# Kernel tuning notes

Hardware: AMD Instinct MI355X
Metric: run time of the kernel (lower is better)

Reference implementation:

```python
import jax, jax.numpy as jnp
import numpy as np

B, T, DIM, H, KV, HD = 1, 2048, 2048, 16, 4, 128


def _rope_tables(T, hd):
    half = hd // 2
    inv_freq = 1.0 / (10000.0 ** (np.arange(0, half, dtype=np.float32) / half))
    t = np.arange(T, dtype=np.float32)
    freqs = np.outer(t, inv_freq)                # [T, hd/2]
    emb = np.concatenate([freqs, freqs], axis=-1)  # [T, hd]
    return jnp.asarray(np.cos(emb)), jnp.asarray(np.sin(emb))


def setup_inputs() -> dict:
    key = jax.random.key(0)
    kx, kq, kk, kv, ko = jax.random.split(key, 5)
    s = 0.02
    x = jax.random.normal(kx, (B, T, DIM), dtype=jnp.float32)
    wq = jax.random.normal(kq, (H * HD, DIM), dtype=jnp.float32) * s
    wk = jax.random.normal(kk, (KV * HD, DIM), dtype=jnp.float32) * s
    wv = jax.random.normal(kv, (KV * HD, DIM), dtype=jnp.float32) * s
    wo = jax.random.normal(ko, (DIM, H * HD), dtype=jnp.float32) * s
    cos, sin = _rope_tables(T, HD)
    return {"x": x, "wq": wq, "wk": wk, "wv": wv, "wo": wo, "cos": cos, "sin": sin}


def _rotate_half(u):
    u1, u2 = jnp.split(u, 2, axis=-1)
    return jnp.concatenate([-u2, u1], axis=-1)


def _apply_rope(u, cos, sin):
    # u: [B, T, h, hd]; cos/sin: [T, hd]
    c = cos[None, :, None, :]
    s = sin[None, :, None, :]
    return u * c + _rotate_half(u) * s


def reference(x, wq, wk, wv, wo, cos, sin):
    b, t, dim = x.shape
    hd = cos.shape[1]
    h = wq.shape[0] // hd
    kvh = wk.shape[0] // hd
    rep = h // kvh
    scale = hd ** -0.5

    q = (x @ wq.T).reshape(b, t, h, hd)
    k = (x @ wk.T).reshape(b, t, kvh, hd)
    v = (x @ wv.T).reshape(b, t, kvh, hd)

    q = _apply_rope(q, cos, sin)
    k = _apply_rope(k, cos, sin)

    # Group queries by shared KV head instead of materializing repeat_kv
    qg = q.reshape(b, t, kvh, rep, hd)
    scores = jnp.einsum('bqgrd,bkgd->bgrqk', qg, k) * scale  # [b,g,r,T,T]
    causal = jnp.tril(jnp.ones((t, t), dtype=bool))
    scores = jnp.where(causal[None, None, None], scores, jnp.float32(-1e30))
    attn = jax.nn.softmax(scores, axis=-1)
    out = jnp.einsum('bgrqk,bkgd->bqgrd', attn, v).reshape(b, t, h * hd)
    return out @ wo.T
```

## Files before the change

### kernel.cpp

```cpp
#include <hip/hip_runtime.h>
#include <hip/hip_bf16.h>

typedef unsigned short u16;
typedef __attribute__((ext_vector_type(8))) short bf16x8;
typedef __attribute__((ext_vector_type(4))) float f32x4;

#define T_SEQ 2048
#define DIM   2048
#define NH    16
#define NKV   4
#define HD    128
#define NQKV  3072
#define SCALE 0.08838834764831845f
#define CHUNK 512

__device__ __forceinline__ u16 f2bf(float f) {
  unsigned int u = __float_as_uint(f);
  unsigned int r = (u + 0x7fffu + ((u >> 16) & 1u)) >> 16;
  return (u16)r;
}
__device__ __forceinline__ float bf2f(u16 v) {
  return __uint_as_float(((unsigned int)v) << 16);
}

#define B1 1048576
#define B2 2097152
#define B3 2359296
#define B4 2621440
#define B5 3670016
__global__ void cast_all(const float4* __restrict__ x,  const float4* __restrict__ wq,
                         const float4* __restrict__ wk, const float4* __restrict__ wv,
                         const float4* __restrict__ wo,
                         ushort4* __restrict__ xb, ushort4* __restrict__ wqkvb,
                         ushort4* __restrict__ wob) {
  int i = blockIdx.x * 256 + threadIdx.x;
  const float4* src; ushort4* dst; int j;
  if (i < B1)      { src = x;  dst = xb;               j = i; }
  else if (i < B2) { src = wq; dst = wqkvb;            j = i - B1; }
  else if (i < B3) { src = wk; dst = wqkvb + 1048576;  j = i - B2; }
  else if (i < B4) { src = wv; dst = wqkvb + 1310720;  j = i - B3; }
  else             { src = wo; dst = wob;              j = i - B4; }
  float4 v = src[j];
  ushort4 o;
  o.x = f2bf(v.x); o.y = f2bf(v.y); o.z = f2bf(v.z); o.w = f2bf(v.w);
  dst[j] = o;
}

#define BM 128
#define BN 128
#define BK 64
#define LDP 72

__global__ __launch_bounds__(256) void gemm_bt(
    const u16* __restrict__ A, const u16* __restrict__ W,
    float* __restrict__ Cf, u16* __restrict__ Cb, int M, int N, int K)
{
  __shared__ u16 As[BM * LDP];
  __shared__ u16 Bs[BN * LDP];
  const int tid  = threadIdx.x;
  const int lane = tid & 63;
  const int wave = tid >> 6;
  const int ln   = lane & 15;
  const int quad = lane >> 4;
  const int m0 = blockIdx.y * BM;
  const int n0 = blockIdx.x * BN;
  const int wm = (wave >> 1) * 64;
  const int wn = (wave & 1) * 64;

  const int sr = tid >> 3;
  const int sc = (tid & 7) * 8;

  f32x4 acc[4][4] = {};

  for (int k0 = 0; k0 < K; k0 += BK) {
#pragma unroll
    for (int c = 0; c < 4; ++c) {
      int row = c * 32 + sr;
      *(bf16x8*)&As[row * LDP + sc] =
          *(const bf16x8*)&A[(size_t)(m0 + row) * K + k0 + sc];
      *(bf16x8*)&Bs[row * LDP + sc] =
          *(const bf16x8*)&W[(size_t)(n0 + row) * K + k0 + sc];
    }
    __syncthreads();
#pragma unroll
    for (int ks = 0; ks < 2; ++ks) {
      bf16x8 af[4], bfr[4];
#pragma unroll
      for (int mt = 0; mt < 4; ++mt)
        af[mt] = *(const bf16x8*)&As[(wm + mt * 16 + ln) * LDP + ks * 32 + quad * 8];
#pragma unroll
      for (int nt = 0; nt < 4; ++nt)
        bfr[nt] = *(const bf16x8*)&Bs[(wn + nt * 16 + ln) * LDP + ks * 32 + quad * 8];
#pragma unroll
      for (int mt = 0; mt < 4; ++mt)
#pragma unroll
        for (int nt = 0; nt < 4; ++nt)
          acc[mt][nt] = __builtin_amdgcn_mfma_f32_16x16x32_bf16(
              af[mt], bfr[nt], acc[mt][nt], 0, 0, 0);
    }
    __syncthreads();
  }

#pragma unroll
  for (int mt = 0; mt < 4; ++mt)
#pragma unroll
    for (int nt = 0; nt < 4; ++nt)
#pragma unroll
      for (int r = 0; r < 4; ++r) {
        int row = m0 + wm + mt * 16 + quad * 4 + r;
        int col = n0 + wn + nt * 16 + ln;
        if (Cb) Cb[(size_t)row * N + col] = f2bf(acc[mt][nt][r]);
        else    Cf[(size_t)row * N + col] = acc[mt][nt][r];
      }
}

__global__ void rope_fused(const u16* __restrict__ QKVb,
                           const float* __restrict__ cosT,
                           const float* __restrict__ sinT,
                           u16* __restrict__ Qs, u16* __restrict__ Kb,
                           u16* __restrict__ Vt)
{
  int b = blockIdx.x, d = threadIdx.x;
  if (b < T_SEQ * NH) {
    int t = b >> 4;
    int h = b & 15;
    const u16* row = QKVb + (size_t)t * NQKV + h * HD;
    float u = bf2f(row[d]);
    float pr = (d < 64) ? -bf2f(row[d + 64]) : bf2f(row[d - 64]);
    float c = cosT[t * HD + d], s = sinT[t * HD + d];
    Qs[(size_t)b * HD + d] = f2bf((u * c + pr * s) * SCALE);
  } else if (b < T_SEQ * (NH + NKV)) {
    int b2 = b - T_SEQ * NH;
    int t = b2 >> 2;
    int g = b2 & 3;
    const u16* row = QKVb + (size_t)t * NQKV + DIM + g * HD;
    float u = bf2f(row[d]);
    float pr = (d < 64) ? -bf2f(row[d + 64]) : bf2f(row[d - 64]);
    float c = cosT[t * HD + d], s = sinT[t * HD + d];
    Kb[(size_t)b2 * HD + d] = f2bf(u * c + pr * s);
  } else {
    int b3 = b - T_SEQ * (NH + NKV);
    int idx = b3 * 128 + d;
    int t  = idx & (T_SEQ - 1);
    int dd = (idx >> 11) & (HD - 1);
    int g  = idx >> 18;
    Vt[idx] = QKVb[(size_t)t * NQKV + DIM + NKV * HD + g * HD + dd];
  }
}

#define KSP 136
#define VSP 72
#define PSP 72
__global__ __launch_bounds__(256) void flash_partial(
    const u16* __restrict__ Qs, const u16* __restrict__ Kb,
    const u16* __restrict__ Vt, u16* __restrict__ Opart,
    float* __restrict__ lpart)
{
  const int c  = blockIdx.x;
  const int qi = blockIdx.y;
  const int h  = blockIdx.z;
  const int b  = qi >> 2;
  if (c > b) return;
  const int g  = h >> 2;
  const int q0 = qi << 7;
  const int k0 = c << 9;
  const int kend = min(k0 + CHUNK, q0 + 128);

  __shared__ u16 Ks[64 * KSP];
  __shared__ u16 Vs[HD * VSP];
  __shared__ u16 Ps[4][16 * PSP];

  const int tid  = threadIdx.x;
  const int lane = tid & 63;
  const int w    = tid >> 6;
  const int ln   = lane & 15;
  const int quad = lane >> 4;

  bf16x8 aq[2][4];
#pragma unroll
  for (int mt = 0; mt < 2; ++mt) {
    const u16* qp = Qs + ((size_t)(q0 + w * 32 + mt * 16 + ln) * NH + h) * HD + quad * 8;
#pragma unroll
    for (int ks = 0; ks < 4; ++ks) aq[mt][ks] = *(const bf16x8*)&qp[ks * 32];
  }

  f32x4 o[2][8] = {};
  float rs[2][4] = {};

  for (int jb = k0; jb < kend; jb += 64) {
    {
      int r = tid >> 4, cc = (tid & 15) * 8;
#pragma unroll
      for (int i = 0; i < 4; ++i) {
        int row = i * 16 + r;
        *(bf16x8*)&Ks[row * KSP + cc] =
            *(const bf16x8*)&Kb[((size_t)(jb + row) * NKV + g) * HD + cc];
      }
    }
    {
      int r = tid >> 3, cc = (tid & 7) * 8;
#pragma unroll
      for (int i = 0; i < 4; ++i) {
        int row = i * 32 + r;
        *(bf16x8*)&Vs[row * VSP + cc] =
            *(const bf16x8*)&Vt[(size_t)(g * HD + row) * T_SEQ + jb + cc];
      }
    }
    __syncthreads();

#pragma unroll
    for (int mt = 0; mt < 2; ++mt) {
      const int rbase = q0 + w * 32 + mt * 16 + quad * 4;
      const int rmax  = q0 + w * 32 + mt * 16 + 15;
      if (jb <= rmax) {
        f32x4 sc[4];
#pragma unroll
        for (int nb = 0; nb < 4; ++nb) {
          f32x4 s = {};
#pragma unroll
          for (int ks = 0; ks < 4; ++ks) {
            bf16x8 kf = *(const bf16x8*)&Ks[(nb * 16 + ln) * KSP + ks * 32 + quad * 8];
            s = __builtin_amdgcn_mfma_f32_16x16x32_bf16(aq[mt][ks], kf, s, 0, 0, 0);
          }
          sc[nb] = s;
        }
        const bool diag = (jb >= q0);
#pragma unroll
        for (int nb = 0; nb < 4; ++nb) {
          int j = jb + nb * 16 + ln;
#pragma unroll
          for (int r = 0; r < 4; ++r) {
            float p = (!diag || j <= rbase + r) ? __expf(sc[nb][r]) : 0.f;
            rs[mt][r] += p;
            Ps[w][(quad * 4 + r) * PSP + nb * 16 + ln] = f2bf(p);
          }
        }
#pragma unroll
        for (int kst = 0; kst < 2; ++kst) {
          bf16x8 ap = *(const bf16x8*)&Ps[w][ln * PSP + kst * 32 + quad * 8];
#pragma unroll
          for (int nb8 = 0; nb8 < 8; ++nb8) {
            bf16x8 bv = *(const bf16x8*)&Vs[(nb8 * 16 + ln) * VSP + kst * 32 + quad * 8];
            o[mt][nb8] = __builtin_amdgcn_mfma_f32_16x16x32_bf16(ap, bv, o[mt][nb8], 0, 0, 0);
          }
        }
      }
    }
    __syncthreads();
  }

  const int slot = h * 40 + 2 * b * (b + 1) + (qi & 3) * (b + 1) + c;
  u16*   op = Opart + (size_t)slot * (128 * 128);
  float* lp = lpart + (size_t)slot * 128;
#pragma unroll
  for (int mt = 0; mt < 2; ++mt) {
#pragma unroll
    for (int r = 0; r < 4; ++r)
#pragma unroll
      for (int off = 1; off < 16; off <<= 1)
        rs[mt][r] += __shfl_xor(rs[mt][r], off);
    int rowb = w * 32 + mt * 16 + quad * 4;
#pragma unroll
    for (int r = 0; r < 4; ++r) {
#pragma unroll
      for (int nb8 = 0; nb8 < 8; ++nb8)
        op[(rowb + r) * 128 + nb8 * 16 + ln] = f2bf(o[mt][nb8][r]);
      if (ln == 0) lp[rowb + r] = rs[mt][r];
    }
  }
}

__global__ void flash_reduce(const u16* __restrict__ Opart,
                             const float* __restrict__ lpart,
                             u16* __restrict__ AO)
{
  const int h = blockIdx.y;
  const int d = threadIdx.x & 127;
  const int t = blockIdx.x * 2 + (threadIdx.x >> 7);
  const int qi = t >> 7, r = t & 127;
  const int b = qi >> 2;
  const int base = h * 40 + 2 * b * (b + 1) + (qi & 3) * (b + 1);
  float so = 0.f, sl = 0.f;
  for (int cc = 0; cc <= b; ++cc) {
    so += bf2f(Opart[(size_t)(base + cc) * (128 * 128) + r * 128 + d]);
    sl += lpart[(size_t)(base + cc) * 128 + r];
  }
  AO[(size_t)t * DIM + h * HD + d] = f2bf(so / sl);
}

extern "C" void kernel_launch(void* const* d_in, const int* in_sizes, int n_in,
                              void* d_out, int out_size, void* d_ws, size_t ws_size,
                              hipStream_t stream) {
  const float* x    = (const float*)d_in[0];
  const float* wq   = (const float*)d_in[1];
  const float* wk   = (const float*)d_in[2];
  const float* wv   = (const float*)d_in[3];
  const float* wo   = (const float*)d_in[4];
  const float* cosT = (const float*)d_in[5];
  const float* sinT = (const float*)d_in[6];
  float* out = (float*)d_out;

  char* ws = (char*)d_ws;
  const size_t MB = 1024 * 1024;
  u16*   xb    = (u16*)(ws + 0 * MB);
  u16*   wqkvb = (u16*)(ws + 8 * MB);
  u16*   wob   = (u16*)(ws + 20 * MB);
  u16*   QKVb  = (u16*)(ws + 28 * MB);
  u16*   Qs    = (u16*)(ws + 8 * MB);
  u16*   Kb    = (u16*)(ws + 16 * MB);
  u16*   Vt    = (u16*)(ws + 18 * MB);
  u16*   AO    = (u16*)(ws + 0 * MB);
  u16*   Opart = (u16*)(ws + 28 * MB);
  float* lpart = (float*)(ws + 48 * MB);

  cast_all<<<B5 / 256, 256, 0, stream>>>(
      (const float4*)x, (const float4*)wq, (const float4*)wk, (const float4*)wv,
      (const float4*)wo, (ushort4*)xb, (ushort4*)wqkvb, (ushort4*)wob);

  gemm_bt<<<dim3(NQKV / BN, T_SEQ / BM), 256, 0, stream>>>(
      xb, wqkvb, nullptr, QKVb, T_SEQ, NQKV, DIM);

  rope_fused<<<T_SEQ * (NH + NKV) + (NKV * HD * T_SEQ) / 128, HD, 0, stream>>>(
      QKVb, cosT, sinT, Qs, Kb, Vt);

  flash_partial<<<dim3(4, 16, 16), 256, 0, stream>>>(Qs, Kb, Vt, Opart, lpart);
  flash_reduce<<<dim3(T_SEQ / 2, NH), 256, 0, stream>>>(Opart, lpart, AO);

  gemm_bt<<<dim3(DIM / BN, T_SEQ / BM), 256, 0, stream>>>(
      AO, wob, out, nullptr, T_SEQ, DIM, DIM);
}
```

Measured before the change: 286.5 us.

## Balance flash-attention splits, swizzle LDS layouts, use direct global-to-LDS GEMM loads

Replaces the fixed 512-key chunking of flash attention with a per-query-tile variable split (61 slots per head, heaviest tiles scheduled first) so that work items are more even and no blocks exit early. K, V and P shared-memory tiles switch from padded rows to XOR-swizzled layouts to avoid bank conflicts. The GEMM stages its tiles with global_load_lds straight into unpadded LDS. The wo cast is split into a separate kernel placed after the QKV GEMM, and workspace offsets are reshuffled, which adds a launch and risks bank conflicts in the now unpadded GEMM LDS reads.

```diff
diff --git a/kernel.cpp b/kernel.cpp
--- a/kernel.cpp
+++ b/kernel.cpp
@@ -12,7 +12,7 @@
 #define HD    128
 #define NQKV  3072
 #define SCALE 0.08838834764831845f
-#define CHUNK 512
+#define NSLOT 61
 
 __device__ __forceinline__ u16 f2bf(float f) {
   unsigned int u = __float_as_uint(f);
@@ -22,41 +22,48 @@
 __device__ __forceinline__ float bf2f(u16 v) {
   return __uint_as_float(((unsigned int)v) << 16);
 }
-
-#define B1 1048576
-#define B2 2097152
-#define B3 2359296
-#define B4 2621440
-#define B5 3670016
-__global__ void cast_all(const float4* __restrict__ x,  const float4* __restrict__ wq,
-                         const float4* __restrict__ wk, const float4* __restrict__ wv,
-                         const float4* __restrict__ wo,
-                         ushort4* __restrict__ xb, ushort4* __restrict__ wqkvb,
-                         ushort4* __restrict__ wob) {
+__device__ __forceinline__ void gload_lds16(const u16* g, u16* l) {
+  __builtin_amdgcn_global_load_lds(
+      (const __attribute__((address_space(1))) unsigned int*)g,
+      (__attribute__((address_space(3))) unsigned int*)l, 16, 0, 0);
+}
+
+#define C1 1048576
+#define C2 2097152
+#define C3 2359296
+#define C4 2621440
+__global__ void cast_main(const float4* __restrict__ x,  const float4* __restrict__ wq,
+                          const float4* __restrict__ wk, const float4* __restrict__ wv,
+                          ushort4* __restrict__ xb, ushort4* __restrict__ wqkvb) {
   int i = blockIdx.x * 256 + threadIdx.x;
   const float4* src; ushort4* dst; int j;
-  if (i < B1)      { src = x;  dst = xb;               j = i; }
-  else if (i < B2) { src = wq; dst = wqkvb;            j = i - B1; }
-  else if (i < B3) { src = wk; dst = wqkvb + 1048576;  j = i - B2; }
-  else if (i < B4) { src = wv; dst = wqkvb + 1310720;  j = i - B3; }
-  else             { src = wo; dst = wob;              j = i - B4; }
+  if (i < C1)      { src = x;  dst = xb;               j = i; }
+  else if (i < C2) { src = wq; dst = wqkvb;            j = i - C1; }
+  else if (i < C3) { src = wk; dst = wqkvb + 1048576;  j = i - C2; }
+  else             { src = wv; dst = wqkvb + 1310720;  j = i - C3; }
   float4 v = src[j];
   ushort4 o;
   o.x = f2bf(v.x); o.y = f2bf(v.y); o.z = f2bf(v.z); o.w = f2bf(v.w);
   dst[j] = o;
 }
+__global__ void cast_wo(const float4* __restrict__ wo, ushort4* __restrict__ wob) {
+  int i = blockIdx.x * 256 + threadIdx.x;
+  float4 v = wo[i];
+  ushort4 o;
+  o.x = f2bf(v.x); o.y = f2bf(v.y); o.z = f2bf(v.z); o.w = f2bf(v.w);
+  wob[i] = o;
+}
 
 #define BM 128
 #define BN 128
 #define BK 64
-#define LDP 72
 
 __global__ __launch_bounds__(256) void gemm_bt(
     const u16* __restrict__ A, const u16* __restrict__ W,
     float* __restrict__ Cf, u16* __restrict__ Cb, int M, int N, int K)
 {
-  __shared__ u16 As[BM * LDP];
-  __shared__ u16 Bs[BN * LDP];
+  __shared__ u16 As[BM * BK];
+  __shared__ u16 Bs[BN * BK];
   const int tid  = threadIdx.x;
   const int lane = tid & 63;
   const int wave = tid >> 6;
@@ -67,19 +74,20 @@
   const int wm = (wave >> 1) * 64;
   const int wn = (wave & 1) * 64;
 
-  const int sr = tid >> 3;
-  const int sc = (tid & 7) * 8;
+  const int srow = wave * 32 + (lane >> 3);
+  const int scol = (lane & 7) * 8;
+  const u16* ga = A + (size_t)(m0 + srow) * K + scol;
+  const u16* gw = W + (size_t)(n0 + srow) * K + scol;
+  u16* la = &As[wave * 32 * BK];
+  u16* lb = &Bs[wave * 32 * BK];
 
   f32x4 acc[4][4] = {};
 
   for (int k0 = 0; k0 < K; k0 += BK) {
 #pragma unroll
-    for (int c = 0; c < 4; ++c) {
-      int row = c * 32 + sr;
-      *(bf16x8*)&As[row * LDP + sc] =
-          *(const bf16x8*)&A[(size_t)(m0 + row) * K + k0 + sc];
-      *(bf16x8*)&Bs[row * LDP + sc] =
-          *(const bf16x8*)&W[(size_t)(n0 + row) * K + k0 + sc];
+    for (int i = 0; i < 4; ++i) {
+      gload_lds16(ga + k0 + (size_t)(i * 8) * K, la + i * 8 * BK);
+      gload_lds16(gw + k0 + (size_t)(i * 8) * K, lb + i * 8 * BK);
     }
     __syncthreads();
 #pragma unroll
@@ -87,10 +95,10 @@
       bf16x8 af[4], bfr[4];
 #pragma unroll
       for (int mt = 0; mt < 4; ++mt)
-        af[mt] = *(const bf16x8*)&As[(wm + mt * 16 + ln) * LDP + ks * 32 + quad * 8];
+        af[mt] = *(const bf16x8*)&As[(wm + mt * 16 + ln) * BK + ks * 32 + quad * 8];
 #pragma unroll
       for (int nt = 0; nt < 4; ++nt)
-        bfr[nt] = *(const bf16x8*)&Bs[(wn + nt * 16 + ln) * LDP + ks * 32 + quad * 8];
+        bfr[nt] = *(const bf16x8*)&Bs[(wn + nt * 16 + ln) * BK + ks * 32 + quad * 8];
 #pragma unroll
       for (int mt = 0; mt < 4; ++mt)
 #pragma unroll
@@ -148,33 +156,48 @@
   }
 }
 
-#define KSP 136
-#define VSP 72
-#define PSP 72
 __global__ __launch_bounds__(256) void flash_partial(
     const u16* __restrict__ Qs, const u16* __restrict__ Kb,
     const u16* __restrict__ Vt, u16* __restrict__ Opart,
     float* __restrict__ lpart)
 {
-  const int c  = blockIdx.x;
-  const int qi = blockIdx.y;
-  const int h  = blockIdx.z;
-  const int b  = qi >> 2;
-  if (c > b) return;
+  __shared__ u16 Ks[64 * 128];
+  __shared__ u16 Vs[128 * 64];
+  __shared__ u16 Ps[4][16 * 64];
+
+  const int srev = 60 - (int)blockIdx.x;
+  const int h = blockIdx.y;
+  int qi, c;
+  if      (srev >= 54) { qi = 15; c = srev - 54; }
+  else if (srev >= 48) { qi = 14; c = srev - 48; }
+  else if (srev >= 42) { qi = 13; c = srev - 42; }
+  else if (srev >= 36) { qi = 12; c = srev - 36; }
+  else if (srev >= 31) { qi = 11; c = srev - 31; }
+  else if (srev >= 26) { qi = 10; c = srev - 26; }
+  else if (srev >= 22) { qi = 9;  c = srev - 22; }
+  else if (srev >= 18) { qi = 8;  c = srev - 18; }
+  else if (srev >= 14) { qi = 7;  c = srev - 14; }
+  else if (srev >= 11) { qi = 6;  c = srev - 11; }
+  else if (srev >= 8)  { qi = 5;  c = srev - 8; }
+  else if (srev >= 6)  { qi = 4;  c = srev - 6; }
+  else if (srev >= 4)  { qi = 3;  c = srev - 4; }
+  else if (srev >= 2)  { qi = 2;  c = srev - 2; }
+  else                 { qi = srev; c = 0; }
+
+  const int nt   = 2 * (qi + 1);
+  const int nc   = (2 * qi + 6) / 5;
+  const int tb   = nt / nc, rem = nt % nc;
+  const int t0   = c * tb + (c < rem ? c : rem);
+  const int tcnt = tb + (c < rem ? 1 : 0);
   const int g  = h >> 2;
   const int q0 = qi << 7;
-  const int k0 = c << 9;
-  const int kend = min(k0 + CHUNK, q0 + 128);
-
-  __shared__ u16 Ks[64 * KSP];
-  __shared__ u16 Vs[HD * VSP];
-  __shared__ u16 Ps[4][16 * PSP];
 
   const int tid  = threadIdx.x;
   const int lane = tid & 63;
   const int w    = tid >> 6;
   const int ln   = lane & 15;
   const int quad = lane >> 4;
+  const int lx   = ln & 7;
 
   bf16x8 aq[2][4];
 #pragma unroll
@@ -187,23 +210,24 @@
   f32x4 o[2][8] = {};
   float rs[2][4] = {};
 
-  for (int jb = k0; jb < kend; jb += 64) {
+  for (int it = t0; it < t0 + tcnt; ++it) {
+    const int jb = it << 6;
     {
-      int r = tid >> 4, cc = (tid & 15) * 8;
+      int r = tid >> 4, ch = tid & 15;
 #pragma unroll
       for (int i = 0; i < 4; ++i) {
         int row = i * 16 + r;
-        *(bf16x8*)&Ks[row * KSP + cc] =
-            *(const bf16x8*)&Kb[((size_t)(jb + row) * NKV + g) * HD + cc];
+        *(bf16x8*)&Ks[row * 128 + ((ch ^ (row & 7)) << 3)] =
+            *(const bf16x8*)&Kb[((size_t)(jb + row) * NKV + g) * HD + ch * 8];
       }
     }
     {
-      int r = tid >> 3, cc = (tid & 7) * 8;
+      int r = tid >> 3, ch = tid & 7;
 #pragma unroll
       for (int i = 0; i < 4; ++i) {
         int row = i * 32 + r;
-        *(bf16x8*)&Vs[row * VSP + cc] =
-            *(const bf16x8*)&Vt[(size_t)(g * HD + row) * T_SEQ + jb + cc];
+        *(bf16x8*)&Vs[row * 64 + ((ch ^ (row & 7)) << 3)] =
+            *(const bf16x8*)&Vt[(size_t)(g * HD + row) * T_SEQ + jb + ch * 8];
       }
     }
     __syncthreads();
@@ -219,7 +243,8 @@
           f32x4 s = {};
 #pragma unroll
           for (int ks = 0; ks < 4; ++ks) {
-            bf16x8 kf = *(const bf16x8*)&Ks[(nb * 16 + ln) * KSP + ks * 32 + quad * 8];
+            bf16x8 kf = *(const bf16x8*)&Ks[(nb * 16 + ln) * 128 +
+                                            ((((ks << 2) + quad) ^ lx) << 3)];
             s = __builtin_amdgcn_mfma_f32_16x16x32_bf16(aq[mt][ks], kf, s, 0, 0, 0);
           }
           sc[nb] = s;
@@ -232,15 +257,17 @@
           for (int r = 0; r < 4; ++r) {
             float p = (!diag || j <= rbase + r) ? __expf(sc[nb][r]) : 0.f;
             rs[mt][r] += p;
-            Ps[w][(quad * 4 + r) * PSP + nb * 16 + ln] = f2bf(p);
+            int prow = quad * 4 + r;
+            Ps[w][prow * 64 + ((((nb << 1) + (ln >> 3)) ^ (prow & 7)) << 3) + (ln & 7)] = f2bf(p);
           }
         }
 #pragma unroll
         for (int kst = 0; kst < 2; ++kst) {
-          bf16x8 ap = *(const bf16x8*)&Ps[w][ln * PSP + kst * 32 + quad * 8];
+          bf16x8 ap = *(const bf16x8*)&Ps[w][ln * 64 + ((((kst << 2) + quad) ^ lx) << 3)];
 #pragma unroll
           for (int nb8 = 0; nb8 < 8; ++nb8) {
-            bf16x8 bv = *(const bf16x8*)&Vs[(nb8 * 16 + ln) * VSP + kst * 32 + quad * 8];
+            bf16x8 bv = *(const bf16x8*)&Vs[(nb8 * 16 + ln) * 64 +
+                                            ((((kst << 2) + quad) ^ lx) << 3)];
             o[mt][nb8] = __builtin_amdgcn_mfma_f32_16x16x32_bf16(ap, bv, o[mt][nb8], 0, 0, 0);
           }
         }
@@ -249,7 +276,7 @@
     __syncthreads();
   }
 
-  const int slot = h * 40 + 2 * b * (b + 1) + (qi & 3) * (b + 1) + c;
+  const int slot = h * NSLOT + srev;
   u16*   op = Opart + (size_t)slot * (128 * 128);
   float* lp = lpart + (size_t)slot * 128;
 #pragma unroll
@@ -278,10 +305,13 @@
   const int d = threadIdx.x & 127;
   const int t = blockIdx.x * 2 + (threadIdx.x >> 7);
   const int qi = t >> 7, r = t & 127;
-  const int b = qi >> 2;
-  const int base = h * 40 + 2 * b * (b + 1) + (qi & 3) * (b + 1);
+  int p = 0;
+#pragma unroll
+  for (int j = 0; j < 16; ++j) p += (j < qi) ? ((2 * j + 6) / 5) : 0;
+  const int nc = (2 * qi + 6) / 5;
+  const int base = h * NSLOT + p;
   float so = 0.f, sl = 0.f;
-  for (int cc = 0; cc <= b; ++cc) {
+  for (int cc = 0; cc < nc; ++cc) {
     so += bf2f(Opart[(size_t)(base + cc) * (128 * 128) + r * 128 + d]);
     sl += lpart[(size_t)(base + cc) * 128 + r];
   }
@@ -304,26 +334,28 @@
   const size_t MB = 1024 * 1024;
   u16*   xb    = (u16*)(ws + 0 * MB);
   u16*   wqkvb = (u16*)(ws + 8 * MB);
-  u16*   wob   = (u16*)(ws + 20 * MB);
-  u16*   QKVb  = (u16*)(ws + 28 * MB);
+  u16*   QKVb  = (u16*)(ws + 20 * MB);
+  u16*   wob   = (u16*)(ws + 0 * MB);
   u16*   Qs    = (u16*)(ws + 8 * MB);
   u16*   Kb    = (u16*)(ws + 16 * MB);
   u16*   Vt    = (u16*)(ws + 18 * MB);
-  u16*   AO    = (u16*)(ws + 0 * MB);
-  u16*   Opart = (u16*)(ws + 28 * MB);
-  float* lpart = (float*)(ws + 48 * MB);
-
-  cast_all<<<B5 / 256, 256, 0, stream>>>(
+  u16*   Opart = (u16*)(ws + 20 * MB);
+  float* lpart = (float*)(ws + 51 * MB);
+  u16*   AO    = (u16*)(ws + 8 * MB);
+
+  cast_main<<<C4 / 256, 256, 0, stream>>>(
       (const float4*)x, (const float4*)wq, (const float4*)wk, (const float4*)wv,
-      (const float4*)wo, (ushort4*)xb, (ushort4*)wqkvb, (ushort4*)wob);
+      (ushort4*)xb, (ushort4*)wqkvb);
 
   gemm_bt<<<dim3(NQKV / BN, T_SEQ / BM), 256, 0, stream>>>(
       xb, wqkvb, nullptr, QKVb, T_SEQ, NQKV, DIM);
 
+  cast_wo<<<(DIM * DIM / 4) / 256, 256, 0, stream>>>((const float4*)wo, (ushort4*)wob);
+
   rope_fused<<<T_SEQ * (NH + NKV) + (NKV * HD * T_SEQ) / 128, HD, 0, stream>>>(
       QKVb, cosT, sinT, Qs, Kb, Vt);
 
-  flash_partial<<<dim3(4, 16, 16), 256, 0, stream>>>(Qs, Kb, Vt, Opart, lpart);
+  flash_partial<<<dim3(NSLOT, NH), 256, 0, stream>>>(Qs, Kb, Vt, Opart, lpart);
   flash_reduce<<<dim3(T_SEQ / 2, NH), 256, 0, stream>>>(Opart, lpart, AO);
 
   gemm_bt<<<dim3(DIM / BN, T_SEQ / BM), 256, 0, stream>>>(
```

Result: no change. 291.1 us (+1.6%).
